# Kernel optimization log

Hardware: AMD Instinct MI355X
Metric: run time of the kernel (lower is better)

The kernel has to match this reference:

```python
import jax, jax.numpy as jnp
import numpy as np

EMBED_DIM = 1024
NUM_HEADS = 16
HEAD_DIM = EMBED_DIM // NUM_HEADS
SCALE = HEAD_DIM ** -0.5


def setup_inputs() -> dict:
    key = jax.random.key(0)
    ks = jax.random.split(key, 11)
    B, SQ, SK = 4, 1024, 2048
    std = EMBED_DIM ** -0.5
    inp = {
        'query': jax.random.normal(ks[0], (B, SQ, EMBED_DIM), jnp.float32),
        'key': jax.random.normal(ks[1], (B, SK, EMBED_DIM), jnp.float32),
        'value': jax.random.normal(ks[2], (B, SK, EMBED_DIM), jnp.float32),
        'Wq': jax.random.normal(ks[3], (EMBED_DIM, EMBED_DIM), jnp.float32) * std,
        'bq': jnp.zeros((EMBED_DIM,), jnp.float32),
        'Wk': jax.random.normal(ks[4], (EMBED_DIM, EMBED_DIM), jnp.float32) * std,
        'bk': jnp.zeros((EMBED_DIM,), jnp.float32),
        'Wv': jax.random.normal(ks[5], (EMBED_DIM, EMBED_DIM), jnp.float32) * std,
        'bv': jnp.zeros((EMBED_DIM,), jnp.float32),
        'Wo': jax.random.normal(ks[6], (EMBED_DIM, EMBED_DIM), jnp.float32) * std,
        'bo': jnp.zeros((EMBED_DIM,), jnp.float32),
    }
    return inp


def reference(query, key, value, Wq, bq, Wk, bk, Wv, bv, Wo, bo):
    B, SQ, _ = query.shape
    SK = key.shape[1]
    # projections (torch Linear: x @ W^T + b)
    q = query @ Wq.T + bq
    k = key @ Wk.T + bk
    v = value @ Wv.T + bv
    # split heads -> [B, H, S, Dh]
    q = q.reshape(B, SQ, NUM_HEADS, HEAD_DIM).transpose(0, 2, 1, 3)
    k = k.reshape(B, SK, NUM_HEADS, HEAD_DIM).transpose(0, 2, 1, 3)
    v = v.reshape(B, SK, NUM_HEADS, HEAD_DIM).transpose(0, 2, 1, 3)
    scores = jnp.einsum('bhqd,bhkd->bhqk', q, k) * SCALE
    attn = jax.nn.softmax(scores, axis=-1)  # dropout p=0 -> identity
    attended = jnp.einsum('bhqk,bhkd->bhqd', attn, v)
    attended = attended.transpose(0, 2, 1, 3).reshape(B, SQ, EMBED_DIM)
    output = attended @ Wo.T + bo
    mean_attn = attn.mean(axis=1)  # average over heads -> [B, SQ, SK]
    return output, mean_attn
```

## Files before the change

### kernel.cpp

```cpp
#include <hip/hip_runtime.h>
#include <hip/hip_bf16.h>
#include <math.h>

#define EMBED 1024
#define NHEADS 16
#define HDIM 64
#define BATCH 4
#define SQL 1024
#define SKL 2048
#define PSC 0.18033688f

typedef unsigned short u16;
typedef __attribute__((ext_vector_type(4))) float f32x4;
typedef __attribute__((ext_vector_type(8))) __bf16 bf16x8;
typedef __attribute__((ext_vector_type(8))) short s16x8;
typedef __attribute__((ext_vector_type(4))) short s16x4;
typedef __attribute__((ext_vector_type(8))) u16 u16x8;

__device__ __forceinline__ u16 f2bf(float x) {
    __hip_bfloat16 h = __float2bfloat16(x);
    return *reinterpret_cast<u16*>(&h);
}
__device__ __forceinline__ float bf2f(u16 u) {
    __hip_bfloat16 h;
    *reinterpret_cast<u16*>(&h) = u;
    return __bfloat162float(h);
}
__device__ __forceinline__ f32x4 mfma16(s16x8 a, s16x8 b, f32x4 c) {
    return __builtin_amdgcn_mfma_f32_16x16x32_bf16(
        __builtin_bit_cast(bf16x8, a), __builtin_bit_cast(bf16x8, b), c, 0, 0, 0);
}
__device__ __forceinline__ f32x4 mfma16k16(s16x4 a, s16x4 b, f32x4 c) {
    return __builtin_amdgcn_mfma_f32_16x16x16bf16_1k(a, b, c, 0, 0, 0);
}
__device__ __forceinline__ void gload16(const void* g, void* l) {
    __builtin_amdgcn_global_load_lds(
        (const __attribute__((address_space(1))) void*)g,
        (__attribute__((address_space(3))) void*)l, 16, 0, 0);
}
__device__ __forceinline__ void stage8k(const char* g, size_t rstrideB,
                                        char* ldsPlane, int w, int lane) {
    int r = w * 8 + (lane >> 3);
    int cs = (lane & 7) ^ (r & 7);
    gload16(g + (size_t)r * rstrideB + cs * 16, ldsPlane + (size_t)w * 1024);
}
#define SBAR() { __builtin_amdgcn_sched_barrier(0); \
    __builtin_amdgcn_s_barrier(); __builtin_amdgcn_sched_barrier(0); }

__global__ __launch_bounds__(256)
void split_w4(const float* __restrict__ Wq, const float* __restrict__ Wk,
              const float* __restrict__ Wv, const float* __restrict__ Wo,
              u16* __restrict__ Wqh, u16* __restrict__ Wkh,
              u16* __restrict__ Wvh, u16* __restrict__ Woh) {
    int bid = blockIdx.x;
    const float* src; u16* dh; u16* dl = nullptr;
    if (bid < 512)       { src = Wq; dh = Wqh; dl = Wqh + 1048576; }
    else if (bid < 1024) { bid -= 512;  src = Wk; dh = Wkh; dl = Wkh + 1048576; }
    else if (bid < 1536) { bid -= 1024; src = Wv; dh = Wvh; }
    else                 { bid -= 1536; src = Wo; dh = Woh; }
    size_t i = ((size_t)bid * 256 + threadIdx.x) * 8;
    float4 a = *(const float4*)&src[i];
    float4 b = *(const float4*)&src[i + 4];
    float v[8] = {a.x, a.y, a.z, a.w, b.x, b.y, b.z, b.w};
    u16x8 hi;
#pragma unroll
    for (int j = 0; j < 8; ++j) hi[j] = f2bf(v[j]);
    *(u16x8*)&dh[i] = hi;
    if (dl) {
        u16x8 lo;
#pragma unroll
        for (int j = 0; j < 8; ++j) lo[j] = f2bf(v[j] - bf2f(hi[j]));
        *(u16x8*)&dl[i] = lo;
    }
}

#define GEMM_LOAD(S, kk) { \
    if constexpr (AMODE == 0) { \
        _Pragma("unroll") for (int j = 0; j < 4; ++j) \
            *(float4*)&ax##S[j * 4] = *(const float4*)&Af[(size_t)(rowBase + srow) * 1024 + (kk) + sc + j * 4]; \
    } else { \
        au##S##0 = *(const u16x8*)&Au[(size_t)(rowBase + srow) * 1024 + (kk) + sc]; \
        au##S##1 = *(const u16x8*)&Au[(size_t)(rowBase + srow) * 1024 + (kk) + sc + 8]; \
    } \
    if constexpr (WMODE == 0) { \
        _Pragma("unroll") for (int j = 0; j < 4; ++j) \
            *(float4*)&bx##S[j * 4] = *(const float4*)&Wf[(size_t)(colBase + srow) * 1024 + (kk) + sc + j * 4]; \
    } else { \
        wh##S##0 = *(const u16x8*)&Wu[(size_t)(colBase + srow) * 1024 + (kk) + sc]; \
        wh##S##1 = *(const u16x8*)&Wu[(size_t)(colBase + srow) * 1024 + (kk) + sc + 8]; \
        if constexpr (WMODE == 2) { \
            wl##S##0 = *(const u16x8*)&Wu[1048576 + (size_t)(colBase + srow) * 1024 + (kk) + sc]; \
            wl##S##1 = *(const u16x8*)&Wu[1048576 + (size_t)(colBase + srow) * 1024 + (kk) + sc + 8]; \
        } \
    } }

#define GEMM_WRITE(S) { \
    u16x8 h0, h1; \
    if constexpr (AMODE == 0) { \
        _Pragma("unroll") for (int j = 0; j < 8; ++j) { \
            h0[j] = f2bf(ax##S[j]); h1[j] = f2bf(ax##S[j + 8]); } \
    } else { h0 = au##S##0; h1 = au##S##1; } \
    *(u16x8*)&sA[srow * 40 + sc] = h0; \
    *(u16x8*)&sA[srow * 40 + sc + 8] = h1; \
    u16x8 b0, b1; \
    if constexpr (WMODE == 0) { \
        _Pragma("unroll") for (int j = 0; j < 8; ++j) { \
            b0[j] = f2bf(bx##S[j]); b1[j] = f2bf(bx##S[j + 8]); } \
    } else { b0 = wh##S##0; b1 = wh##S##1; } \
    *(u16x8*)&sB[0][srow * 40 + sc] = b0; \
    *(u16x8*)&sB[0][srow * 40 + sc + 8] = b1; \
    if constexpr (WMODE == 2) { \
        *(u16x8*)&sB[1][srow * 40 + sc] = wl##S##0; \
        *(u16x8*)&sB[1][srow * 40 + sc + 8] = wl##S##1; \
    } }

#define GEMM_COMPUTE() { \
    s16x8 afh[4], bfh[4], bfl[4]; \
    _Pragma("unroll") for (int mi = 0; mi < 4; ++mi) { \
        int ai = (wm * 64 + mi * 16 + (lane & 15)) * 40 + (lane >> 4) * 8; \
        afh[mi] = *(const s16x8*)&sA[ai]; \
    } \
    _Pragma("unroll") for (int ni = 0; ni < 4; ++ni) { \
        int bi = (wn * 64 + ni * 16 + (lane & 15)) * 40 + (lane >> 4) * 8; \
        bfh[ni] = *(const s16x8*)&sB[0][bi]; \
        if constexpr (WMODE == 2) bfl[ni] = *(const s16x8*)&sB[1][bi]; \
    } \
    _Pragma("unroll") for (int mi = 0; mi < 4; ++mi) \
        _Pragma("unroll") for (int ni = 0; ni < 4; ++ni) { \
            acc[mi][ni] = mfma16(afh[mi], bfh[ni], acc[mi][ni]); \
            if constexpr (WMODE == 2) \
                acc[mi][ni] = mfma16(afh[mi], bfl[ni], acc[mi][ni]); \
        } }

template<int AMODE, int WMODE, int OUT_MODE>
__global__ __launch_bounds__(256)
void gemm_mfma(const void* __restrict__ Ap, const void* __restrict__ Wop,
               const float* __restrict__ bias, void* __restrict__ Y0p,
               int M, int N, int bshift) {
    __shared__ u16 sA[128 * 40];
    __shared__ u16 sB[2][128 * 40];

    const int t = threadIdx.x;
    const int lane = t & 63;
    const int w = t >> 6;
    const int wm = w >> 1, wn = w & 1;
    const int rowBase = blockIdx.y * 128;
    const int colBase = blockIdx.x * 128;
    const int srow = t >> 1;
    const int sc = (t & 1) * 16;

    const float* Af = (const float*)Ap;
    const u16* Au = (const u16*)Ap;
    const float* Wf = (const float*)Wop;
    const u16* Wu = (const u16*)Wop;

    f32x4 acc[4][4];
#pragma unroll
    for (int i = 0; i < 4; ++i)
#pragma unroll
        for (int j = 0; j < 4; ++j) acc[i][j] = (f32x4){0.f, 0.f, 0.f, 0.f};

    float ax0[16], ax1[16], bx0[16], bx1[16];
    u16x8 au00, au01, au10, au11;
    u16x8 wh00, wh01, wl00, wl01, wh10, wh11, wl10, wl11;

    GEMM_LOAD(0, 0)
    GEMM_LOAD(1, 32)

    for (int k0 = 0; k0 < 1024; k0 += 64) {
        __syncthreads();
        GEMM_WRITE(0)
        __syncthreads();
        if (k0 + 64 < 1024) GEMM_LOAD(0, k0 + 64)
        GEMM_COMPUTE()
        __syncthreads();
        GEMM_WRITE(1)
        __syncthreads();
        if (k0 + 96 < 1024) GEMM_LOAD(1, k0 + 96)
        GEMM_COMPUTE()
    }

#pragma unroll
    for (int mi = 0; mi < 4; ++mi)
#pragma unroll
        for (int ni = 0; ni < 4; ++ni)
#pragma unroll
            for (int rr = 0; rr < 4; ++rr) {
                int mg = rowBase + wm * 64 + mi * 16 + (lane >> 4) * 4 + rr;
                int ng = colBase + wn * 64 + ni * 16 + (lane & 15);
                float y = acc[mi][ni][rr];
                if constexpr (OUT_MODE == 0) {
                    ((float*)Y0p)[(size_t)mg * N + ng] = y + bias[ng];
                } else if constexpr (OUT_MODE == 4) {
                    y += bias[mg];
                    size_t idx = ((size_t)((ng >> 11) * 16 + (mg >> 6)) * 64 + (mg & 63)) * 2048 + (ng & 2047);
                    ((u16*)Y0p)[idx] = f2bf(y);
                } else if constexpr (OUT_MODE == 5) {
                    y += bias[ng];
                    int bb = mg >> bshift, s = mg & ((1 << bshift) - 1);
                    size_t idx = ((((size_t)(bb * 16 + (ng >> 6))) << bshift) + s) * 64 + (ng & 63);
                    ((u16*)Y0p)[idx] = f2bf(y);
                }
            }
}

__global__ __launch_bounds__(512, 4)
void attn_O(const u16* __restrict__ Qhi, const u16* __restrict__ Khi,
            const u16* __restrict__ VT, u16* __restrict__ Att,
            float* __restrict__ llog) {
    __shared__ char lds[49152];
    float* sOf = (float*)lds;
    float* sL2 = (float*)(lds + 35840);

    const int t = threadIdx.x;
    const int w = t >> 6, lane = t & 63;
    const int g = lane >> 4, c16 = lane & 15;
    const int qt = blockIdx.x >> 6;
    const int g6 = blockIdx.x & 63;
    const int b = g6 >> 4, h = g6 & 15;
    const int qbase = qt * 128;
    const int wq = w >> 1, wk = w & 1;
    const int kswz = (g ^ (c16 & 7)) << 4;
    const int vsw0 = (((wk * 4 + 0 + (g >> 1)) ^ (c16 & 7)) << 4) | ((g & 1) << 3);
    const int vsw1 = (((wk * 4 + 2 + (g >> 1)) ^ (c16 & 7)) << 4) | ((g & 1) << 3);

    const char* Kh_g = (const char*)(Khi + (size_t)(b * 16 + h) * SKL * 64);
    const char* V_g  = (const char*)(VT + (size_t)(b * 16 + h) * 64 * SKL);

    s16x8 qh[2][2];
    const size_t qrowbase = (size_t)(b * 16 + h) * SQL + qbase;
#pragma unroll
    for (int qf = 0; qf < 2; ++qf) {
        size_t qo = (qrowbase + wq * 32 + qf * 16 + c16) * 64 + g * 8;
        qh[qf][0] = *(const s16x8*)&Qhi[qo];
        qh[qf][1] = *(const s16x8*)&Qhi[qo + 32];
    }

    stage8k(Kh_g, 128, lds, w, lane);
    stage8k(V_g, 4096, lds + 24576, w, lane);
    stage8k(Kh_g + 8192, 128, lds + 8192, w, lane);
    stage8k(V_g + 128, 4096, lds + 24576 + 8192, w, lane);

    f32x4 oacc[2][4];
#pragma unroll
    for (int qf = 0; qf < 2; ++qf)
#pragma unroll
        for (int i = 0; i < 4; ++i) oacc[qf][i] = (f32x4){0.f, 0.f, 0.f, 0.f};
    float lsum[2] = {0.f, 0.f};

    int cur = 0;
    for (int c = 0; c < 32; ++c) {
        if (c < 31) { asm volatile("s_waitcnt vmcnt(2)" ::: "memory"); }
        else        { asm volatile("s_waitcnt vmcnt(0)" ::: "memory"); }
        SBAR();
        if (c + 2 < 32) {
            int nb = cur + 2; if (nb >= 3) nb -= 3;
            stage8k(Kh_g + (size_t)(c + 2) * 8192, 128, lds + nb * 8192, w, lane);
            stage8k(V_g + (size_t)(c + 2) * 128, 4096, lds + 24576 + nb * 8192, w, lane);
        }
        char* curK = lds + cur * 8192;
        char* curV = lds + 24576 + cur * 8192;
#pragma unroll
        for (int kf = 0; kf < 2; ++kf) {
            int kb = (wk * 32 + kf * 16 + c16) * 128 + kswz;
            s16x8 kh0 = *(const s16x8*)(curK + kb);
            s16x8 kh1 = *(const s16x8*)(curK + (kb ^ 64));
            s16x4 pb[2];
#pragma unroll
            for (int qf = 0; qf < 2; ++qf) {
                f32x4 s = {0.f, 0.f, 0.f, 0.f};
                s = mfma16(kh0, qh[qf][0], s);
                s = mfma16(kh1, qh[qf][1], s);
                float e0 = exp2f(s[0] * PSC);
                float e1 = exp2f(s[1] * PSC);
                float e2 = exp2f(s[2] * PSC);
                float e3 = exp2f(s[3] * PSC);
                lsum[qf] += (e0 + e1) + (e2 + e3);
                pb[qf][0] = (short)f2bf(e0); pb[qf][1] = (short)f2bf(e1);
                pb[qf][2] = (short)f2bf(e2); pb[qf][3] = (short)f2bf(e3);
            }
            int vs = kf ? vsw1 : vsw0;
#pragma unroll
            for (int df = 0; df < 4; ++df) {
                s16x4 vf = *(const s16x4*)(curV + (df * 16 + c16) * 128 + vs);
                oacc[0][df] = mfma16k16(vf, pb[0], oacc[0][df]);
                oacc[1][df] = mfma16k16(vf, pb[1], oacc[1][df]);
            }
        }
        ++cur; if (cur == 3) cur = 0;
    }

#pragma unroll
    for (int qf = 0; qf < 2; ++qf) {
        lsum[qf] += __shfl_xor(lsum[qf], 16, 64);
        lsum[qf] += __shfl_xor(lsum[qf], 32, 64);
    }
    __syncthreads();
#pragma unroll
    for (int qf = 0; qf < 2; ++qf)
        if (g == 0) sL2[wk * 128 + wq * 32 + qf * 16 + c16] = lsum[qf];

#pragma unroll
    for (int half = 0; half < 2; ++half) {
        if (half) __syncthreads();
        if ((wq >> 1) == half) {
            int qlocal = (wq & 1) * 32 + c16;
#pragma unroll
            for (int qf = 0; qf < 2; ++qf)
#pragma unroll
                for (int df = 0; df < 4; ++df)
#pragma unroll
                    for (int r = 0; r < 4; ++r)
                        sOf[wk * 4352 + (df * 16 + g * 4 + r) * 68 + qlocal + qf * 16] =
                            oacc[qf][df][r];
        }
        __syncthreads();
        {
            int q = t >> 3, dg = t & 7;
            float l = sL2[half * 64 + q] + sL2[128 + half * 64 + q];
            float linv = 1.f / l;
            u16x8 ov;
#pragma unroll
            for (int i = 0; i < 8; ++i) {
                int d = dg * 8 + i;
                ov[i] = f2bf((sOf[d * 68 + q] + sOf[4352 + d * 68 + q]) * linv);
            }
            *(u16x8*)&Att[(size_t)(b * SQL + qbase + half * 64 + q) * EMBED + h * 64 + dg * 8] = ov;
            if (dg == 0)
                llog[(size_t)(b * 16 + h) * SQL + qbase + half * 64 + q] = log2f(l);
        }
    }
}

__global__ __launch_bounds__(512, 4)
void attn_mean(const u16* __restrict__ Qhi, const u16* __restrict__ Khi,
               const float* __restrict__ llog, float* __restrict__ meanOut) {
    __shared__ char lds[81920];

    const int t = threadIdx.x;
    const int w = t >> 6, lane = t & 63;
    const int g = lane >> 4, c16 = lane & 15;
    const int qt = blockIdx.x >> 6;
    const int low = blockIdx.x & 63;
    const int b = low >> 4, ks = low & 15;
    const int qbase = qt * 128;
    const int kbase = ks * 128;
    const int wq = w >> 1, wk = w & 1;
    const int kswz = (g ^ (c16 & 7)) << 4;

    const size_t QH_STRIDE = (size_t)SQL * 128;
    const size_t KH_STRIDE = (size_t)SKL * 128;
    const char* Qh_b = (const char*)(Qhi + ((size_t)(b * 16) * SQL + qbase) * 64);
    const char* Kh_b = (const char*)(Khi + ((size_t)(b * 16) * SKL + kbase) * 64);
    const float* ll_b = llog + (size_t)(b * 16) * SQL + qbase;

    f32x4 ma[2][4];
#pragma unroll
    for (int qf = 0; qf < 2; ++qf)
#pragma unroll
        for (int i = 0; i < 4; ++i) ma[qf][i] = (f32x4){0.f, 0.f, 0.f, 0.f};

    stage8k(Qh_b, 128, lds, w, lane);
    stage8k(Qh_b + 8192, 128, lds + 8192, w, lane);
    float lbA0 = ll_b[wq * 32 + c16];
    float lbA1 = ll_b[wq * 32 + 16 + c16];
    stage8k(Kh_b, 128, lds + 32768, w, lane);
    stage8k(Kh_b + 8192, 128, lds + 32768 + 8192, w, lane);
    stage8k(Qh_b + QH_STRIDE, 128, lds + 16384, w, lane);
    stage8k(Qh_b + QH_STRIDE + 8192, 128, lds + 16384 + 8192, w, lane);
    float lbB0 = ll_b[SQL + wq * 32 + c16];
    float lbB1 = ll_b[SQL + wq * 32 + 16 + c16];
    stage8k(Kh_b + KH_STRIDE, 128, lds + 32768 + 16384, w, lane);
    stage8k(Kh_b + KH_STRIDE + 8192, 128, lds + 32768 + 16384 + 8192, w, lane);

    int curK = 0;
    for (int h = 0; h < 16; ++h) {
        if (h < 15) { asm volatile("s_waitcnt vmcnt(4)" ::: "memory"); }
        else        { asm volatile("s_waitcnt vmcnt(0)" ::: "memory"); }
        SBAR();

        const char* sQ = lds + (h & 1) * 16384;
        s16x8 qa0, qa1, qc0, qc1;
        {
            int qb0 = (wq * 32 + c16) * 128 + kswz;
            qa0 = *(const s16x8*)(sQ + qb0);
            qa1 = *(const s16x8*)(sQ + (qb0 ^ 64));
            int qb1 = (wq * 32 + 16 + c16) * 128 + kswz;
            qc0 = *(const s16x8*)(sQ + qb1);
            qc1 = *(const s16x8*)(sQ + (qb1 ^ 64));
        }
        asm volatile("s_waitcnt lgkmcnt(0)" ::: "memory");
        SBAR();

        float lb0 = lbA0, lb1 = lbA1;
        lbA0 = lbB0; lbA1 = lbB1;

        if (h + 2 < 16) {
            const char* Qg = Qh_b + (size_t)(h + 2) * QH_STRIDE;
            char* qdst = lds + (h & 1) * 16384;
            stage8k(Qg, 128, qdst, w, lane);
            stage8k(Qg + 8192, 128, qdst + 8192, w, lane);
            lbB0 = ll_b[(size_t)(h + 2) * SQL + wq * 32 + c16];
            lbB1 = ll_b[(size_t)(h + 2) * SQL + wq * 32 + 16 + c16];
            const char* Kg = Kh_b + (size_t)(h + 2) * KH_STRIDE;
            int nb = curK + 2; if (nb >= 3) nb -= 3;
            char* kdst = lds + 32768 + nb * 16384;
            stage8k(Kg, 128, kdst, w, lane);
            stage8k(Kg + 8192, 128, kdst + 8192, w, lane);
        }

        const char* sK = lds + 32768 + curK * 16384;
#pragma unroll
        for (int kf = 0; kf < 4; ++kf) {
            int kb = (kf * 32 + wk * 16 + c16) * 128 + kswz;
            s16x8 kh0 = *(const s16x8*)(sK + kb);
            s16x8 kh1 = *(const s16x8*)(sK + (kb ^ 64));
            {
                f32x4 s = {0.f, 0.f, 0.f, 0.f};
                s = mfma16(kh0, qa0, s);
                s = mfma16(kh1, qa1, s);
                ma[0][kf][0] += exp2f(s[0] * PSC - lb0);
                ma[0][kf][1] += exp2f(s[1] * PSC - lb0);
                ma[0][kf][2] += exp2f(s[2] * PSC - lb0);
                ma[0][kf][3] += exp2f(s[3] * PSC - lb0);
            }
            {
                f32x4 s = {0.f, 0.f, 0.f, 0.f};
                s = mfma16(kh0, qc0, s);
                s = mfma16(kh1, qc1, s);
                ma[1][kf][0] += exp2f(s[0] * PSC - lb1);
                ma[1][kf][1] += exp2f(s[1] * PSC - lb1);
                ma[1][kf][2] += exp2f(s[2] * PSC - lb1);
                ma[1][kf][3] += exp2f(s[3] * PSC - lb1);
            }
        }
        ++curK; if (curK == 3) curK = 0;
    }

    const float s16c = 1.f / 16.f;
#pragma unroll
    for (int qf = 0; qf < 2; ++qf)
#pragma unroll
        for (int kf = 0; kf < 4; ++kf) {
            f32x4 m = ma[qf][kf];
            m[0] *= s16c; m[1] *= s16c; m[2] *= s16c; m[3] *= s16c;
            *(f32x4*)&meanOut[(size_t)(b * SQL + qbase + wq * 32 + qf * 16 + c16) * SKL +
                              kbase + kf * 32 + wk * 16 + g * 4] = m;
        }
}

extern "C" void kernel_launch(void* const* d_in, const int* in_sizes, int n_in,
                              void* d_out, int out_size, void* d_ws, size_t ws_size,
                              hipStream_t stream) {
    const float* query = (const float*)d_in[0];
    const float* key   = (const float*)d_in[1];
    const float* value = (const float*)d_in[2];
    const float* Wq = (const float*)d_in[3];
    const float* bq = (const float*)d_in[4];
    const float* Wk = (const float*)d_in[5];
    const float* bk = (const float*)d_in[6];
    const float* Wv = (const float*)d_in[7];
    const float* bv = (const float*)d_in[8];
    const float* Wo = (const float*)d_in[9];
    const float* bo = (const float*)d_in[10];

    float* out = (float*)d_out;
    float* meanOut = out + (size_t)BATCH * SQL * EMBED;

    u16* Qhi = (u16*)d_ws;
    u16* Khi = Qhi + (size_t)4096 * 1024;
    u16* VTh = Khi + (size_t)8192 * 1024;
    u16* Att = VTh + (size_t)8192 * 1024;
    float* llog = (float*)(Att + (size_t)4096 * 1024);
    u16* Wqh = (u16*)(llog + 64 * 1024);
    u16* Wkh = Wqh + (size_t)2 * 1024 * 1024;
    u16* Wvh = Wkh + (size_t)2 * 1024 * 1024;
    u16* Woh = Wvh + (size_t)1024 * 1024;

    split_w4<<<dim3(2048), 256, 0, stream>>>(Wq, Wk, Wv, Wo, Wqh, Wkh, Wvh, Woh);

    gemm_mfma<0, 2, 5><<<dim3(8, 32), 256, 0, stream>>>(query, Wqh, bq, Qhi, 4096, 1024, 10);
    gemm_mfma<0, 2, 5><<<dim3(8, 64), 256, 0, stream>>>(key, Wkh, bk, Khi, 8192, 1024, 11);
    gemm_mfma<1, 0, 4><<<dim3(64, 8), 256, 0, stream>>>(Wvh, value, bv, VTh, 1024, 8192, 0);

    attn_O<<<dim3(512), dim3(512), 0, stream>>>(Qhi, Khi, VTh, Att, llog);
    attn_mean<<<dim3(512), dim3(512), 0, stream>>>(Qhi, Khi, llog, meanOut);

    gemm_mfma<1, 1, 0><<<dim3(8, 32), 256, 0, stream>>>(Att, Woh, bo, out, 4096, 1024, 0);
}
```

Before: 245.4 us.

## Drop hi/lo weight split, fold softmax scale into Q, sum P via MFMA

Removes the bf16 hi/lo residual split for Wq and Wk, so the Q and K projections use a single bf16 weight and half the MFMAs and LDS traffic. The softmax scale is folded into the Q projection epilogue before rounding to bf16, which removes the per-element multiply in both attention kernels. Row sums of P are now computed with an MFMA against a ones vector instead of scalar adds and cross-lane shuffles. This lowers precision of the Q/K projections and of the pre-scaled Q, and the row sum now uses the bf16-rounded P values.

Result: faster. 228.5 us (-6.9%).

```diff
diff --git a/kernel.cpp b/kernel.cpp
--- a/kernel.cpp
+++ b/kernel.cpp
@@ -48,14 +48,14 @@
     __builtin_amdgcn_s_barrier(); __builtin_amdgcn_sched_barrier(0); }
 
 __global__ __launch_bounds__(256)
-void split_w4(const float* __restrict__ Wq, const float* __restrict__ Wk,
-              const float* __restrict__ Wv, const float* __restrict__ Wo,
-              u16* __restrict__ Wqh, u16* __restrict__ Wkh,
-              u16* __restrict__ Wvh, u16* __restrict__ Woh) {
+void cvt_w(const float* __restrict__ Wq, const float* __restrict__ Wk,
+           const float* __restrict__ Wv, const float* __restrict__ Wo,
+           u16* __restrict__ Wqh, u16* __restrict__ Wkh,
+           u16* __restrict__ Wvh, u16* __restrict__ Woh) {
     int bid = blockIdx.x;
-    const float* src; u16* dh; u16* dl = nullptr;
-    if (bid < 512)       { src = Wq; dh = Wqh; dl = Wqh + 1048576; }
-    else if (bid < 1024) { bid -= 512;  src = Wk; dh = Wkh; dl = Wkh + 1048576; }
+    const float* src; u16* dh;
+    if (bid < 512)       { src = Wq; dh = Wqh; }
+    else if (bid < 1024) { bid -= 512;  src = Wk; dh = Wkh; }
     else if (bid < 1536) { bid -= 1024; src = Wv; dh = Wvh; }
     else                 { bid -= 1536; src = Wo; dh = Woh; }
     size_t i = ((size_t)bid * 256 + threadIdx.x) * 8;
@@ -66,12 +66,6 @@
 #pragma unroll
     for (int j = 0; j < 8; ++j) hi[j] = f2bf(v[j]);
     *(u16x8*)&dh[i] = hi;
-    if (dl) {
-        u16x8 lo;
-#pragma unroll
-        for (int j = 0; j < 8; ++j) lo[j] = f2bf(v[j] - bf2f(hi[j]));
-        *(u16x8*)&dl[i] = lo;
-    }
 }
 
 #define GEMM_LOAD(S, kk) { \
@@ -88,10 +82,6 @@
     } else { \
         wh##S##0 = *(const u16x8*)&Wu[(size_t)(colBase + srow) * 1024 + (kk) + sc]; \
         wh##S##1 = *(const u16x8*)&Wu[(size_t)(colBase + srow) * 1024 + (kk) + sc + 8]; \
-        if constexpr (WMODE == 2) { \
-            wl##S##0 = *(const u16x8*)&Wu[1048576 + (size_t)(colBase + srow) * 1024 + (kk) + sc]; \
-            wl##S##1 = *(const u16x8*)&Wu[1048576 + (size_t)(colBase + srow) * 1024 + (kk) + sc + 8]; \
-        } \
     } }
 
 #define GEMM_WRITE(S) { \
@@ -107,30 +97,22 @@
         _Pragma("unroll") for (int j = 0; j < 8; ++j) { \
             b0[j] = f2bf(bx##S[j]); b1[j] = f2bf(bx##S[j + 8]); } \
     } else { b0 = wh##S##0; b1 = wh##S##1; } \
-    *(u16x8*)&sB[0][srow * 40 + sc] = b0; \
-    *(u16x8*)&sB[0][srow * 40 + sc + 8] = b1; \
-    if constexpr (WMODE == 2) { \
-        *(u16x8*)&sB[1][srow * 40 + sc] = wl##S##0; \
-        *(u16x8*)&sB[1][srow * 40 + sc + 8] = wl##S##1; \
-    } }
+    *(u16x8*)&sB[srow * 40 + sc] = b0; \
+    *(u16x8*)&sB[srow * 40 + sc + 8] = b1; }
 
 #define GEMM_COMPUTE() { \
-    s16x8 afh[4], bfh[4], bfl[4]; \
+    s16x8 afh[4], bfh[4]; \
     _Pragma("unroll") for (int mi = 0; mi < 4; ++mi) { \
         int ai = (wm * 64 + mi * 16 + (lane & 15)) * 40 + (lane >> 4) * 8; \
         afh[mi] = *(const s16x8*)&sA[ai]; \
     } \
     _Pragma("unroll") for (int ni = 0; ni < 4; ++ni) { \
         int bi = (wn * 64 + ni * 16 + (lane & 15)) * 40 + (lane >> 4) * 8; \
-        bfh[ni] = *(const s16x8*)&sB[0][bi]; \
-        if constexpr (WMODE == 2) bfl[ni] = *(const s16x8*)&sB[1][bi]; \
+        bfh[ni] = *(const s16x8*)&sB[bi]; \
     } \
     _Pragma("unroll") for (int mi = 0; mi < 4; ++mi) \
-        _Pragma("unroll") for (int ni = 0; ni < 4; ++ni) { \
-            acc[mi][ni] = mfma16(afh[mi], bfh[ni], acc[mi][ni]); \
-            if constexpr (WMODE == 2) \
-                acc[mi][ni] = mfma16(afh[mi], bfl[ni], acc[mi][ni]); \
-        } }
+        _Pragma("unroll") for (int ni = 0; ni < 4; ++ni) \
+            acc[mi][ni] = mfma16(afh[mi], bfh[ni], acc[mi][ni]); }
 
 template<int AMODE, int WMODE, int OUT_MODE>
 __global__ __launch_bounds__(256)
@@ -138,7 +120,7 @@
                const float* __restrict__ bias, void* __restrict__ Y0p,
                int M, int N, int bshift) {
     __shared__ u16 sA[128 * 40];
-    __shared__ u16 sB[2][128 * 40];
+    __shared__ u16 sB[128 * 40];
 
     const int t = threadIdx.x;
     const int lane = t & 63;
@@ -162,7 +144,7 @@
 
     float ax0[16], ax1[16], bx0[16], bx1[16];
     u16x8 au00, au01, au10, au11;
-    u16x8 wh00, wh01, wl00, wl01, wh10, wh11, wl10, wl11;
+    u16x8 wh00, wh01, wh10, wh11;
 
     GEMM_LOAD(0, 0)
     GEMM_LOAD(1, 32)
@@ -195,8 +177,9 @@
                     y += bias[mg];
                     size_t idx = ((size_t)((ng >> 11) * 16 + (mg >> 6)) * 64 + (mg & 63)) * 2048 + (ng & 2047);
                     ((u16*)Y0p)[idx] = f2bf(y);
-                } else if constexpr (OUT_MODE == 5) {
+                } else if constexpr (OUT_MODE == 5 || OUT_MODE == 6) {
                     y += bias[ng];
+                    if constexpr (OUT_MODE == 6) y *= PSC;
                     int bb = mg >> bshift, s = mg & ((1 << bshift) - 1);
                     size_t idx = ((((size_t)(bb * 16 + (ng >> 6))) << bshift) + s) * 64 + (ng & 63);
                     ((u16*)Y0p)[idx] = f2bf(y);
@@ -241,12 +224,15 @@
     stage8k(Kh_g + 8192, 128, lds + 8192, w, lane);
     stage8k(V_g + 128, 4096, lds + 24576 + 8192, w, lane);
 
+    const s16x4 onesf = {(short)0x3F80, (short)0x3F80, (short)0x3F80, (short)0x3F80};
     f32x4 oacc[2][4];
-#pragma unroll
-    for (int qf = 0; qf < 2; ++qf)
+    f32x4 lacc[2];
+#pragma unroll
+    for (int qf = 0; qf < 2; ++qf) {
+        lacc[qf] = (f32x4){0.f, 0.f, 0.f, 0.f};
 #pragma unroll
         for (int i = 0; i < 4; ++i) oacc[qf][i] = (f32x4){0.f, 0.f, 0.f, 0.f};
-    float lsum[2] = {0.f, 0.f};
+    }
 
     int cur = 0;
     for (int c = 0; c < 32; ++c) {
@@ -271,13 +257,11 @@
                 f32x4 s = {0.f, 0.f, 0.f, 0.f};
                 s = mfma16(kh0, qh[qf][0], s);
                 s = mfma16(kh1, qh[qf][1], s);
-                float e0 = exp2f(s[0] * PSC);
-                float e1 = exp2f(s[1] * PSC);
-                float e2 = exp2f(s[2] * PSC);
-                float e3 = exp2f(s[3] * PSC);
-                lsum[qf] += (e0 + e1) + (e2 + e3);
-                pb[qf][0] = (short)f2bf(e0); pb[qf][1] = (short)f2bf(e1);
-                pb[qf][2] = (short)f2bf(e2); pb[qf][3] = (short)f2bf(e3);
+                pb[qf][0] = (short)f2bf(exp2f(s[0]));
+                pb[qf][1] = (short)f2bf(exp2f(s[1]));
+                pb[qf][2] = (short)f2bf(exp2f(s[2]));
+                pb[qf][3] = (short)f2bf(exp2f(s[3]));
+                lacc[qf] = mfma16k16(onesf, pb[qf], lacc[qf]);
             }
             int vs = kf ? vsw1 : vsw0;
 #pragma unroll
@@ -290,15 +274,10 @@
         ++cur; if (cur == 3) cur = 0;
     }
 
-#pragma unroll
-    for (int qf = 0; qf < 2; ++qf) {
-        lsum[qf] += __shfl_xor(lsum[qf], 16, 64);
-        lsum[qf] += __shfl_xor(lsum[qf], 32, 64);
-    }
     __syncthreads();
 #pragma unroll
     for (int qf = 0; qf < 2; ++qf)
-        if (g == 0) sL2[wk * 128 + wq * 32 + qf * 16 + c16] = lsum[qf];
+        if (g == 0) sL2[wk * 128 + wq * 32 + qf * 16 + c16] = lacc[qf][0];
 
 #pragma unroll
     for (int half = 0; half < 2; ++half) {
@@ -419,19 +398,19 @@
                 f32x4 s = {0.f, 0.f, 0.f, 0.f};
                 s = mfma16(kh0, qa0, s);
                 s = mfma16(kh1, qa1, s);
-                ma[0][kf][0] += exp2f(s[0] * PSC - lb0);
-                ma[0][kf][1] += exp2f(s[1] * PSC - lb0);
-                ma[0][kf][2] += exp2f(s[2] * PSC - lb0);
-                ma[0][kf][3] += exp2f(s[3] * PSC - lb0);
+                ma[0][kf][0] += exp2f(s[0] - lb0);
+                ma[0][kf][1] += exp2f(s[1] - lb0);
+                ma[0][kf][2] += exp2f(s[2] - lb0);
+                ma[0][kf][3] += exp2f(s[3] - lb0);
             }
             {
                 f32x4 s = {0.f, 0.f, 0.f, 0.f};
                 s = mfma16(kh0, qc0, s);
                 s = mfma16(kh1, qc1, s);
-                ma[1][kf][0] += exp2f(s[0] * PSC - lb1);
-                ma[1][kf][1] += exp2f(s[1] * PSC - lb1);
-                ma[1][kf][2] += exp2f(s[2] * PSC - lb1);
-                ma[1][kf][3] += exp2f(s[3] * PSC - lb1);
+                ma[1][kf][0] += exp2f(s[0] - lb1);
+                ma[1][kf][1] += exp2f(s[1] - lb1);
+                ma[1][kf][2] += exp2f(s[2] - lb1);
+                ma[1][kf][3] += exp2f(s[3] - lb1);
             }
         }
         ++curK; if (curK == 3) curK = 0;
@@ -473,14 +452,14 @@
     u16* Att = VTh + (size_t)8192 * 1024;
     float* llog = (float*)(Att + (size_t)4096 * 1024);
     u16* Wqh = (u16*)(llog + 64 * 1024);
-    u16* Wkh = Wqh + (size_t)2 * 1024 * 1024;
-    u16* Wvh = Wkh + (size_t)2 * 1024 * 1024;
+    u16* Wkh = Wqh + (size_t)1024 * 1024;
+    u16* Wvh = Wkh + (size_t)1024 * 1024;
     u16* Woh = Wvh + (size_t)1024 * 1024;
 
-    split_w4<<<dim3(2048), 256, 0, stream>>>(Wq, Wk, Wv, Wo, Wqh, Wkh, Wvh, Woh);
-
-    gemm_mfma<0, 2, 5><<<dim3(8, 32), 256, 0, stream>>>(query, Wqh, bq, Qhi, 4096, 1024, 10);
-    gemm_mfma<0, 2, 5><<<dim3(8, 64), 256, 0, stream>>>(key, Wkh, bk, Khi, 8192, 1024, 11);
+    cvt_w<<<dim3(2048), 256, 0, stream>>>(Wq, Wk, Wv, Wo, Wqh, Wkh, Wvh, Woh);
+
+    gemm_mfma<0, 1, 6><<<dim3(8, 32), 256, 0, stream>>>(query, Wqh, bq, Qhi, 4096, 1024, 10);
+    gemm_mfma<0, 1, 5><<<dim3(8, 64), 256, 0, stream>>>(key, Wkh, bk, Khi, 8192, 1024, 11);
     gemm_mfma<1, 0, 4><<<dim3(64, 8), 256, 0, stream>>>(Wvh, value, bv, VTh, 1024, 8192, 0);
 
     attn_O<<<dim3(512), dim3(512), 0, stream>>>(Qhi, Khi, VTh, Att, llog);
```
